# Performance work log

Hardware: AMD Instinct MI355X
Metric: run time of the kernel (lower is better)

Reference implementation:

```python
import jax, jax.numpy as jnp
import numpy as np

B, S_IN, T_OUT, H, L, V = 64, 512, 64, 1024, 2, 1024


def setup_inputs() -> dict:
    key = jax.random.key(0)
    ks = iter(jax.random.split(key, 64))
    def p(shape, scale=0.02):
        return (jax.random.normal(next(ks), shape, jnp.float32) * scale)
    d = {"x": jax.random.normal(next(ks), (B, 2, S_IN), jnp.float32)}
    d["emb"] = p((V, H))
    for l in range(L):
        i = 2 if l == 0 else H
        d[f"enc_Wih{l}"] = p((3 * H, i)); d[f"enc_Whh{l}"] = p((3 * H, H))
        d[f"enc_bih{l}"] = p((3 * H,));   d[f"enc_bhh{l}"] = p((3 * H,))
        d[f"dec_Wih{l}"] = p((H, H));     d[f"dec_Whh{l}"] = p((H, H))
        d[f"dec_bih{l}"] = p((H,));       d[f"dec_bhh{l}"] = p((H,))
    d["hq_W"] = p((H, H)); d["hq_b"] = p((H,))
    d["comb_W"] = p((H, 2 * H)); d["comb_b"] = p((H,))
    d["fc_W"] = p((V, H)); d["fc_b"] = p((V,))
    return d


def _gru_layer(x_seq, Wih, Whh, bih, bhh):
    # x_seq: [B,T,I] -> (outputs [B,T,H], h_T [B,H]). PyTorch GRU gate order r,z,n.
    xp = jnp.einsum('bti,gi->btg', x_seq, Wih) + bih  # [B,T,3H]
    h0 = jnp.zeros((x_seq.shape[0], Whh.shape[1]), x_seq.dtype)
    def step(h, xpt):
        hp = h @ Whh.T + bhh
        xr, xz, xn = jnp.split(xpt, 3, axis=-1)
        hr, hz, hn = jnp.split(hp, 3, axis=-1)
        r = jax.nn.sigmoid(xr + hr)
        z = jax.nn.sigmoid(xz + hz)
        n = jnp.tanh(xn + r * hn)
        h = (1.0 - z) * n + z * h
        return h, h
    hT, ys = jax.lax.scan(step, h0, jnp.swapaxes(xp, 0, 1))
    return jnp.swapaxes(ys, 0, 1), hT


def _forward(x, emb,
             enc_Wih0, enc_Whh0, enc_bih0, enc_bhh0,
             enc_Wih1, enc_Whh1, enc_bih1, enc_bhh1,
             dec_Wih0, dec_Whh0, dec_bih0, dec_bhh0,
             dec_Wih1, dec_Whh1, dec_bih1, dec_bhh1,
             hq_W, hq_b, comb_W, comb_b, fc_W, fc_b):
    enc_params = [(enc_Wih0, enc_Whh0, enc_bih0, enc_bhh0),
                  (enc_Wih1, enc_Whh1, enc_bih1, enc_bhh1)]
    dec_params = [(dec_Wih0, dec_Whh0, dec_bih0, dec_bhh0),
                  (dec_Wih1, dec_Whh1, dec_bih1, dec_bhh1)]
    # ---- encoder: GRU over x permuted to [B, S_in, 2] ----
    seq = jnp.transpose(x, (0, 2, 1)).astype(jnp.float32)
    h_enc = []
    for (Wih, Whh, bih, bhh) in enc_params:
        seq, hT = _gru_layer(seq, Wih, Whh, bih, bhh)
        h_enc.append(hT)
    enc_outs = seq                      # [B, S_in, H]
    hidden0 = jnp.stack(h_enc, axis=0)  # [L, B, H]

    tok0 = jnp.zeros((B,), jnp.int32)
    def dec_step(carry, _):
        tok, hid = carry
        inp = emb[tok]                  # [B, H]
        new_h = []
        for l, (Wih, Whh, bih, bhh) in enumerate(dec_params):
            h = jnp.tanh(inp @ Wih.T + bih + hid[l] @ Whh.T + bhh)
            new_h.append(h)
            inp = h
        hid = jnp.stack(new_h, axis=0)
        q = inp @ hq_W.T + hq_b                          # [B, H]
        scores = jnp.einsum('bsh,bh->bs', enc_outs, q)   # [B, S_in]
        aw = jax.nn.softmax(scores, axis=1)
        att = jnp.einsum('bs,bsh->bh', aw, enc_outs)     # [B, H]
        logits = jnp.concatenate([inp, att], axis=-1) @ comb_W.T + comb_b
        logits = logits @ fc_W.T + fc_b                  # [B, V]
        tok = jnp.argmax(logits, axis=-1).astype(jnp.int32)
        return (tok, hid), (logits, aw)
    (_, hidden), (logits_t, aw_t) = jax.lax.scan(dec_step, (tok0, hidden0), None, length=T_OUT)
    vec_out = jnp.swapaxes(logits_t, 0, 1)   # [B, T_out, V]
    attn = aw_t[-1][:, None, :]              # [B, 1, S_in] (last step, as in source)
    return vec_out, hidden, attn


def reference(x, emb,
              enc_Wih0, enc_Whh0, enc_bih0, enc_bhh0,
              enc_Wih1, enc_Whh1, enc_bih1, enc_bhh1,
              dec_Wih0, dec_Whh0, dec_bih0, dec_bhh0,
              dec_Wih1, dec_Whh1, dec_bih1, dec_bhh1,
              hq_W, hq_b, comb_W, comb_b, fc_W, fc_b):
    return _forward(x, emb,
                    enc_Wih0, enc_Whh0, enc_bih0, enc_bhh0,
                    enc_Wih1, enc_Whh1, enc_bih1, enc_bhh1,
                    dec_Wih0, dec_Whh0, dec_bih0, dec_bhh0,
                    dec_Wih1, dec_Whh1, dec_bih1, dec_bhh1,
                    hq_W, hq_b, comb_W, comb_b, fc_W, fc_b)
```

## Files before the change

kernel.cpp:

```cpp
#include <hip/hip_runtime.h>
#include <stdint.h>


#define BB 64
#define SS 512
#define TT 64
#define HH 1024
#define VV 1024
#define BH 65536
#define SH 524288
#define OFF_HID  4194304
#define OFF_ATTN 4325376

typedef _Float16 half8  __attribute__((ext_vector_type(8)));
typedef float    floatx4 __attribute__((ext_vector_type(4)));

struct P {
  const float *x, *emb;
  const float *eWih0, *eWhh0, *ebih0, *ebhh0;
  const float *dWih0, *dWhh0, *dbih0, *dbhh0;
  const float *eWih1, *eWhh1, *ebih1, *ebhh1;
  const float *dWih1, *dWhh1, *dbih1, *dbhh1;
  const float *hqW, *hqb, *combW, *combb, *fcW, *fcb;
  uint32_t* enc_i;
  _Float16 *W0h,*W0l;
  _Float16 *W1h,*W1l;
  _Float16 *embh,*embl,*T0h,*T0l;
  _Float16 *wih0dh,*wih0dl,*wih1dh,*wih1dl,*whh0dh,*whh0dl,*whh1dh,*whh1dl;
  _Float16 *hqh,*hql,*combh,*combl,*fch,*fcl;
  _Float16 *h0h,*h0l,*h1h,*h1l;
  _Float16 *dh0h,*dh0l,*dh1h,*dh1l;
  _Float16 *cath,*catl;
  _Float16 *ch,*cl;
  float *u0,*u1,*w1x,*q;
  float *attp_o;
  float *attp_ml;
  float *sc63;
  unsigned long long* amax;
  float* dout;
};

struct GSet { const _Float16 *Wh, *Wl, *Ah, *Al; const float *bias; float *out; };

__device__ __forceinline__ void splitf(float x, _Float16& hi, _Float16& lo){
  _Float16 h = (_Float16)x; hi = h;
  lo = (_Float16)((x - (float)h) * 2048.0f);
}
__device__ __forceinline__ float reconf(_Float16 hi, _Float16 lo){
  return fmaf((float)lo, 1.0f/2048.0f, (float)hi);
}
__device__ __forceinline__ float recon_u32(uint32_t w){
  float hi = (float)__builtin_bit_cast(_Float16, (unsigned short)(w & 0xffffu));
  float lo = (float)__builtin_bit_cast(_Float16, (unsigned short)(w >> 16));
  return fmaf(lo, 1.0f/2048.0f, hi);
}
__device__ __forceinline__ uint32_t pack_pair(float x){
  _Float16 hi, lo; splitf(x, hi, lo);
  return (uint32_t)__builtin_bit_cast(unsigned short, hi)
       | ((uint32_t)__builtin_bit_cast(unsigned short, lo) << 16);
}
__device__ __forceinline__ unsigned ordf(float f){
  unsigned u = __float_as_uint(f);
  return (u & 0x80000000u) ? ~u : (u | 0x80000000u);
}

template<int NT, int KH, bool SPLIT>
__device__ __forceinline__ void gemm_core(
    const _Float16* __restrict__ Ah0, const _Float16* __restrict__ Al0,
    const _Float16* __restrict__ Ah1, const _Float16* __restrict__ Al1,
    int sA,
    const _Float16* __restrict__ Wh, const _Float16* __restrict__ Wl,
    int nrows, _Float16* ldsW, float* accOut)
{
  const int tid = threadIdx.x, lane = tid & 63, wave = tid >> 6;
  const int mA = (wave<<4) + (lane & 15);
  const int kb = ((lane>>4) << 3);
  const int wstride = KH << 10;
  floatx4 aH[NT], aM1[NT], aM2[NT];
  int ne[NT];
  const _Float16* bh_base[NT];
  const _Float16* bl_base[NT];
  #pragma unroll
  for (int nt=0; nt<NT; ++nt){
    int nn = (lane & 15) + (nt<<4);
    ne[nt] = nn < nrows ? nn : nrows - 1;
    bh_base[nt] = ldsW + ne[nt]*1032 + kb;
    aH[nt]  = floatx4{0.f,0.f,0.f,0.f};
    aM1[nt] = floatx4{0.f,0.f,0.f,0.f};
    aM2[nt] = floatx4{0.f,0.f,0.f,0.f};
  }
  #pragma unroll
  for (int kh=0; kh<KH; ++kh){
    __syncthreads();
    const int iters = (nrows*128 + 255) >> 8;
    for (int it=0; it<iters; ++it){
      int idx = tid + (it<<8);
      int row = idx >> 7, col = (idx & 127) << 3;
      if (row < nrows)
        *(half8*)(ldsW + row*1032 + col) =
            *(const half8*)(Wh + row*wstride + (kh<<10) + col);
    }
    __syncthreads();
    const _Float16* ah_p = ((KH==2 && kh==1) ? Ah1 : Ah0) + mA*sA + kb;
    const _Float16* al_p = ((KH==2 && kh==1) ? Al1 : Al0) + mA*sA + kb;
    #pragma unroll
    for (int nt=0; nt<NT; ++nt) bl_base[nt] = Wl + ne[nt]*wstride + (kh<<10) + kb;
    #pragma unroll 4
    for (int ks=0; ks<32; ++ks){
      half8 ah = *(const half8*)(ah_p + (ks<<5));
      half8 al = *(const half8*)(al_p + (ks<<5));
      #pragma unroll
      for (int nt=0; nt<NT; ++nt){
        half8 bh = *(const half8*)(bh_base[nt] + (ks<<5));
        half8 bl = *(const half8*)(bl_base[nt] + (ks<<5));
        aH[nt]  = __builtin_amdgcn_mfma_f32_16x16x32_f16(ah, bh, aH[nt],  0,0,0);
        aM1[nt] = __builtin_amdgcn_mfma_f32_16x16x32_f16(ah, bl, aM1[nt], 0,0,0);
        aM2[nt] = __builtin_amdgcn_mfma_f32_16x16x32_f16(al, bh, aM2[nt], 0,0,0);
      }
    }
    if (SPLIT){
      #pragma unroll
      for (int nt=0; nt<NT; ++nt){
        #pragma unroll
        for (int r=0;r<4;++r)
          accOut[(kh*NT + nt)*4 + r] = aH[nt][r] + (aM1[nt][r] + aM2[nt][r]) * (1.f/2048.f);
        aH[nt]  = floatx4{0.f,0.f,0.f,0.f};
        aM1[nt] = floatx4{0.f,0.f,0.f,0.f};
        aM2[nt] = floatx4{0.f,0.f,0.f,0.f};
      }
    }
  }
  if (!SPLIT){
    #pragma unroll
    for (int nt=0; nt<NT; ++nt)
      #pragma unroll
      for (int r=0;r<4;++r)
        accOut[nt*4 + r] = aH[nt][r] + (aM1[nt][r] + aM2[nt][r]) * (1.f/2048.f);
  }
}

__global__ __launch_bounds__(256) void k_split(const float* __restrict__ src,
                                               _Float16* dh, _Float16* dl, int n){
  for (int i = blockIdx.x*256 + threadIdx.x; i < n; i += gridDim.x*256){
    _Float16 hi,lo; splitf(src[i],hi,lo); dh[i]=hi; dl[i]=lo;
  }
}

__global__ __launch_bounds__(256) void k_rw0(P p){
  const int n = 128*24*1024;
  for (int i = blockIdx.x*256 + threadIdx.x; i < n; i += gridDim.x*256){
    int k = i & 1023; int rest = i >> 10; int rr = rest % 24; int blk = rest / 24;
    int grow = (rr>>3)*1024 + (blk<<3) + (rr&7);
    _Float16 hi,lo; splitf(p.eWhh0[grow*1024 + k],hi,lo);
    p.W0h[i]=hi; p.W0l[i]=lo;
  }
}
__global__ __launch_bounds__(256) void k_rw1(P p){
  const int n = 128*24*2048;
  for (int i = blockIdx.x*256 + threadIdx.x; i < n; i += gridDim.x*256){
    int k = i & 2047; int rest = i >> 11; int rr = rest % 24; int blk = rest / 24;
    int grow = (rr>>3)*1024 + (blk<<3) + (rr&7);
    float v = (k < 1024) ? p.eWhh1[grow*1024 + k] : p.eWih1[grow*1024 + (k-1024)];
    _Float16 hi,lo; splitf(v,hi,lo);
    p.W1h[i]=hi; p.W1l[i]=lo;
  }
}
__global__ __launch_bounds__(256) void k_zero(P p){
  int i = blockIdx.x*256 + threadIdx.x;
  p.h1h[i] = (_Float16)0.f; p.h1l[i] = (_Float16)0.f;
  p.h0h[BH + i] = (_Float16)0.f; p.h0l[BH + i] = (_Float16)0.f;
}
__global__ __launch_bounds__(256) void k_t0(P p){
  __shared__ _Float16 ldsW[16*1032];
  const int ns = blockIdx.x & 63, mc = blockIdx.x >> 6;
  float acc[4];
  gemm_core<1,1,false>(p.embh + mc*65536, p.embl + mc*65536, nullptr, nullptr, 1024,
                       p.wih0dh + ns*16*1024, p.wih0dl + ns*16*1024, 16, ldsW, acc);
  const int lane = threadIdx.x & 63, wave = threadIdx.x >> 6;
  const int n = lane & 15, col = (ns<<4) + n;
  const float bv = p.dbih0[col];
  #pragma unroll
  for (int r=0;r<4;++r){
    int v = mc*64 + (wave<<4) + ((lane>>4)<<2) + r;
    _Float16 hi,lo; splitf(acc[r] + bv, hi, lo);
    p.T0h[v*1024 + col] = hi; p.T0l[v*1024 + col] = lo;
  }
}

__global__ __launch_bounds__(256) void k_enc(P p, int e){
  const int tid = threadIdx.x, lane = tid & 63, wave = tid >> 6;
  const bool is0 = blockIdx.x < 128;
  if (is0 && e >= 512) return;
  if (!is0 && e < 1) return;
  const int blk = is0 ? blockIdx.x : blockIdx.x - 128;
  const int j0 = blk << 3;

  __shared__ _Float16 ldsW[24*1032];
  __shared__ float ldsG[2][24][68];
  __shared__ float ldsC[24][4];

  if (tid < 24){
    int grow = (tid>>3)*1024 + j0 + (tid & 7);
    if (is0){
      ldsC[tid][0] = p.eWih0[grow*2+0];
      ldsC[tid][1] = p.eWih0[grow*2+1];
      ldsC[tid][2] = p.ebih0[grow];
      ldsC[tid][3] = p.ebhh0[grow];
    } else {
      ldsC[tid][0] = p.ebih1[grow];
      ldsC[tid][1] = p.ebhh1[grow];
    }
  }

  const int cur = e & 1, prv = cur ^ 1;
  float acc[16];
  if (is0){
    gemm_core<2,1,true>(p.h0h + prv*BH, p.h0l + prv*BH, nullptr, nullptr, 1024,
                        p.W0h + blk*24*1024, p.W0l + blk*24*1024, 24, ldsW, acc);
    #pragma unroll
    for (int nt=0; nt<2; ++nt){
      int n = (lane & 15) + (nt<<4);
      if (n < 24){
        #pragma unroll
        for (int r=0;r<4;++r)
          ldsG[0][n][(wave<<4)+((lane>>4)<<2)+r] = acc[nt*4+r];
      }
    }
  } else {
    gemm_core<2,2,true>(p.h1h + prv*BH, p.h1l + prv*BH,
                        p.h0h + prv*BH, p.h0l + prv*BH, 1024,
                        p.W1h + blk*24*2048, p.W1l + blk*24*2048, 24, ldsW, acc);
    #pragma unroll
    for (int kh=0; kh<2; ++kh){
      #pragma unroll
      for (int nt=0; nt<2; ++nt){
        int n = (lane & 15) + (nt<<4);
        if (n < 24){
          #pragma unroll
          for (int r=0;r<4;++r)
            ldsG[kh][n][(wave<<4)+((lane>>4)<<2)+r] = acc[(kh*2+nt)*4+r];
        }
      }
    }
  }
  __syncthreads();

  #pragma unroll
  for (int it=0; it<2; ++it){
    int idx = tid + (it<<8);
    int b = idx & 63, j = idx >> 6;
    int col = j0 + j;
    if (is0){
      int t = e;
      float hr = ldsG[0][j][b]    + ldsC[j][3];
      float hz = ldsG[0][8+j][b]  + ldsC[8+j][3];
      float hn = ldsG[0][16+j][b] + ldsC[16+j][3];
      float x0 = p.x[b*1024 + t], x1 = p.x[b*1024 + 512 + t];
      float xr = fmaf(x0, ldsC[j][0],    fmaf(x1, ldsC[j][1],    ldsC[j][2]));
      float xz = fmaf(x0, ldsC[8+j][0],  fmaf(x1, ldsC[8+j][1],  ldsC[8+j][2]));
      float xn = fmaf(x0, ldsC[16+j][0], fmaf(x1, ldsC[16+j][1], ldsC[16+j][2]));
      float rg = 1.0f/(1.0f + expf(-(xr+hr)));
      float zg = 1.0f/(1.0f + expf(-(xz+hz)));
      float ng = tanhf(xn + rg*hn);
      float hold = reconf(p.h0h[prv*BH + b*1024 + col], p.h0l[prv*BH + b*1024 + col]);
      float hnew = (1.0f - zg)*ng + zg*hold;
      _Float16 hi,lo; splitf(hnew,hi,lo);
      p.h0h[cur*BH + b*1024 + col] = hi;
      p.h0l[cur*BH + b*1024 + col] = lo;
    } else {
      int t = e - 1;
      float hr = ldsG[0][j][b]    + ldsC[j][1];
      float hz = ldsG[0][8+j][b]  + ldsC[8+j][1];
      float hn = ldsG[0][16+j][b] + ldsC[16+j][1];
      float xr = ldsG[1][j][b]    + ldsC[j][0];
      float xz = ldsG[1][8+j][b]  + ldsC[8+j][0];
      float xn = ldsG[1][16+j][b] + ldsC[16+j][0];
      float rg = 1.0f/(1.0f + expf(-(xr+hr)));
      float zg = 1.0f/(1.0f + expf(-(xz+hz)));
      float ng = tanhf(xn + rg*hn);
      float hold = reconf(p.h1h[prv*BH + b*1024 + col], p.h1l[prv*BH + b*1024 + col]);
      float hnew = (1.0f - zg)*ng + zg*hold;
      _Float16 hi,lo; splitf(hnew,hi,lo);
      p.h1h[cur*BH + b*1024 + col] = hi;
      p.h1l[cur*BH + b*1024 + col] = lo;
      p.enc_i[b*SH + t*1024 + col] = pack_pair(hnew);
    }
  }
}

__global__ __launch_bounds__(256) void k_dgemm2(GSet a, GSet b){
  const int tid = threadIdx.x, lane = tid & 63, wave = tid >> 6;
  const GSet g = blockIdx.x < 128 ? a : b;
  const int blk = blockIdx.x & 127;
  __shared__ _Float16 ldsW[8*1032];
  float acc[4];
  gemm_core<1,1,false>(g.Ah, g.Al, nullptr, nullptr, 1024,
                       g.Wh + blk*8*1024, g.Wl + blk*8*1024, 8, ldsW, acc);
  int n = lane & 15;
  if (n < 8){
    int col = (blk<<3) + n;
    float bv = g.bias[col];
    #pragma unroll
    for (int r=0;r<4;++r){
      int m = (wave<<4)+((lane>>4)<<2)+r;
      g.out[m*1024 + col] = acc[r] + bv;
    }
  }
}

__global__ __launch_bounds__(256) void k_dec0(P p, int t){
  const int tid = threadIdx.x, b = blockIdx.x;
  __shared__ unsigned long long red[256];
  unsigned long long v = 0;
  if (t > 0 && tid < 128) v = p.amax[b*128 + tid];
  red[tid] = v; __syncthreads();
  for (int off=128; off>=1; off>>=1){
    if (tid < off){ unsigned long long o = red[tid+off]; if (o > red[tid]) red[tid] = o; }
    __syncthreads();
  }
  const int tokb = (t > 0) ? (1023 - (int)(red[0] & 0xffffffffULL)) : 0;
  #pragma unroll
  for (int i=0;i<4;++i){
    int h = tid + (i<<8);
    float val = tanhf(reconf(p.T0h[tokb*1024+h], p.T0l[tokb*1024+h]) + p.u0[b*1024+h]);
    _Float16 hi,lo; splitf(val,hi,lo);
    p.dh0h[b*1024+h]=hi; p.dh0l[b*1024+h]=lo;
  }
}
__global__ __launch_bounds__(256) void k_dec2(P p){
  const int tid = threadIdx.x, b = blockIdx.x;
  #pragma unroll
  for (int i=0;i<4;++i){
    int h = tid + (i<<8);
    float val = tanhf(p.w1x[b*1024+h] + p.u1[b*1024+h]);
    _Float16 hi,lo; splitf(val,hi,lo);
    p.dh1h[b*1024+h]=hi; p.dh1l[b*1024+h]=lo;
    p.cath[b*2048+h]=hi; p.catl[b*2048+h]=lo;
  }
}
__global__ __launch_bounds__(256) void k_flash(P p, int t){
  const int tid = threadIdx.x, lane = tid & 63, wave = tid >> 6;
  const int b = blockIdx.x >> 1, half = blockIdx.x & 1;
  const int s0 = half << 8;
  const bool last = (t == 63);
  float qv[16];
  #pragma unroll
  for (int i=0;i<16;++i) qv[i] = p.q[b*1024 + (i<<6) + lane];
  float ov[16];
  #pragma unroll
  for (int i=0;i<16;++i) ov[i] = 0.f;
  float mrun = -3.0e38f, lrun = 0.f;
  for (int si=0; si<64; ++si){
    int s = s0 + (wave<<6) + si;
    const uint32_t* ep = p.enc_i + b*SH + s*1024 + lane;
    float ef[16]; float partial = 0.f;
    #pragma unroll
    for (int i=0;i<16;++i){
      ef[i] = recon_u32(ep[i<<6]);
      partial = fmaf(ef[i], qv[i], partial);
    }
    #pragma unroll
    for (int off=32; off; off>>=1) partial += __shfl_xor(partial, off, 64);
    if (last && lane == 0) p.sc63[b*512 + s] = partial;
    float mnew = fmaxf(mrun, partial);
    float fac = __expf(mrun - mnew);
    float w   = __expf(partial - mnew);
    lrun = fmaf(lrun, fac, w);
    #pragma unroll
    for (int i=0;i<16;++i) ov[i] = fmaf(ov[i], fac, w*ef[i]);
    mrun = mnew;
  }
  __shared__ float ldsO[4][1024];
  __shared__ float ldsM[4], ldsL2[4];
  #pragma unroll
  for (int i=0;i<16;++i) ldsO[wave][(i<<6)+lane] = ov[i];
  if (lane == 0){ ldsM[wave] = mrun; ldsL2[wave] = lrun; }
  __syncthreads();
  float M = fmaxf(fmaxf(ldsM[0],ldsM[1]), fmaxf(ldsM[2],ldsM[3]));
  float f0 = __expf(ldsM[0]-M), f1 = __expf(ldsM[1]-M),
        f2 = __expf(ldsM[2]-M), f3 = __expf(ldsM[3]-M);
  if (tid == 0){
    p.attp_ml[b*4 + half*2 + 0] = M;
    p.attp_ml[b*4 + half*2 + 1] = f0*ldsL2[0] + f1*ldsL2[1] + f2*ldsL2[2] + f3*ldsL2[3];
  }
  #pragma unroll
  for (int i=0;i<4;++i){
    int h = tid + (i<<8);
    p.attp_o[(b*2+half)*1024 + h] =
        f0*ldsO[0][h] + f1*ldsO[1][h] + f2*ldsO[2][h] + f3*ldsO[3][h];
  }
}
__global__ __launch_bounds__(256) void k_dec5(P p, int t){
  const int tid = threadIdx.x, b = blockIdx.x;
  float m0 = p.attp_ml[b*4+0], l0 = p.attp_ml[b*4+1];
  float m1 = p.attp_ml[b*4+2], l1 = p.attp_ml[b*4+3];
  float M = fmaxf(m0,m1);
  float f0 = expf(m0-M), f1 = expf(m1-M);
  float invL = 1.0f/(f0*l0 + f1*l1);
  #pragma unroll
  for (int i=0;i<4;++i){
    int h = tid + (i<<8);
    float o = (f0*p.attp_o[(b*2+0)*1024+h] + f1*p.attp_o[(b*2+1)*1024+h]) * invL;
    _Float16 hi,lo; splitf(o,hi,lo);
    p.cath[b*2048 + 1024 + h] = hi; p.catl[b*2048 + 1024 + h] = lo;
  }
  if (t == 63){
    #pragma unroll
    for (int i=0;i<2;++i){
      int s = tid + (i<<8);
      p.dout[OFF_ATTN + b*512 + s] = expf(p.sc63[b*512+s] - M) * invL;
    }
  }
}
__global__ __launch_bounds__(256) void k_comb(P p){
  const int tid = threadIdx.x, lane = tid & 63, wave = tid >> 6;
  const int blk = blockIdx.x;
  __shared__ _Float16 ldsW[8*1032];
  float acc[4];
  gemm_core<1,2,false>(p.cath, p.catl, p.cath + 1024, p.catl + 1024, 2048,
                       p.combh + blk*8*2048, p.combl + blk*8*2048, 8, ldsW, acc);
  int n = lane & 15;
  if (n < 8){
    int col = (blk<<3) + n;
    float bv = p.combb[col];
    #pragma unroll
    for (int r=0;r<4;++r){
      int m = (wave<<4)+((lane>>4)<<2)+r;
      _Float16 hi,lo; splitf(acc[r] + bv, hi, lo);
      p.ch[m*1024 + col] = hi; p.cl[m*1024 + col] = lo;
    }
  }
}
__global__ __launch_bounds__(256) void k_fc(P p, int t){
  const int tid = threadIdx.x, lane = tid & 63, wave = tid >> 6;
  const int blk = blockIdx.x;
  __shared__ _Float16 ldsW[8*1032];
  __shared__ float ldsL[8][68];
  float acc[4];
  gemm_core<1,1,false>(p.ch, p.cl, nullptr, nullptr, 1024,
                       p.fch + blk*8*1024, p.fcl + blk*8*1024, 8, ldsW, acc);
  int n = lane & 15;
  if (n < 8){
    int col = (blk<<3) + n;
    float bv = p.fcb[col];
    #pragma unroll
    for (int r=0;r<4;++r){
      int m = (wave<<4)+((lane>>4)<<2)+r;
      float val = acc[r] + bv;
      p.dout[m*65536 + t*1024 + col] = val;
      ldsL[n][m] = val;
    }
  }
  __syncthreads();
  if (tid < 64){
    int b = tid; float best = -3.0e38f; int bi = 0;
    #pragma unroll
    for (int jj=0; jj<8; ++jj){
      float v = ldsL[jj][b];
      if (v > best){ best = v; bi = jj; }
    }
    unsigned long long pk = ((unsigned long long)ordf(best) << 32)
                          | (unsigned)(1023 - ((blk<<3) + bi));
    p.amax[b*128 + blk] = pk;
  }
}
__global__ __launch_bounds__(256) void k_hidden(P p){
  int idx = blockIdx.x*256 + threadIdx.x;
  int i = idx & 65535;
  float v = (idx >> 16) ? reconf(p.dh1h[i], p.dh1l[i]) : reconf(p.dh0h[i], p.dh0l[i]);
  p.dout[OFF_HID + idx] = v;
}

extern "C" void kernel_launch(void* const* d_in, const int* in_sizes, int n_in,
                              void* d_out, int out_size, void* d_ws, size_t ws_size,
                              hipStream_t stream)
{
  (void)in_sizes; (void)n_in; (void)out_size;
  P p;
  p.x     = (const float*)d_in[0];  p.emb   = (const float*)d_in[1];
  p.eWih0 = (const float*)d_in[2];  p.eWhh0 = (const float*)d_in[3];
  p.ebih0 = (const float*)d_in[4];  p.ebhh0 = (const float*)d_in[5];
  p.dWih0 = (const float*)d_in[6];  p.dWhh0 = (const float*)d_in[7];
  p.dbih0 = (const float*)d_in[8];  p.dbhh0 = (const float*)d_in[9];
  p.eWih1 = (const float*)d_in[10]; p.eWhh1 = (const float*)d_in[11];
  p.ebih1 = (const float*)d_in[12]; p.ebhh1 = (const float*)d_in[13];
  p.dWih1 = (const float*)d_in[14]; p.dWhh1 = (const float*)d_in[15];
  p.dbih1 = (const float*)d_in[16]; p.dbhh1 = (const float*)d_in[17];
  p.hqW   = (const float*)d_in[18]; p.hqb   = (const float*)d_in[19];
  p.combW = (const float*)d_in[20]; p.combb = (const float*)d_in[21];
  p.fcW   = (const float*)d_in[22]; p.fcb   = (const float*)d_in[23];
  p.dout  = (float*)d_out;

  char* base = (char*)d_ws; size_t off = 0;
  auto alloc = [&](size_t bytes)->char*{
    char* r = base + off; off = (off + bytes + 255) & ~(size_t)255; return r;
  };
  p.enc_i = (uint32_t*)alloc(33554432ULL*4);
  p.W0h = (_Float16*)alloc(3145728ULL*2);  p.W0l = (_Float16*)alloc(3145728ULL*2);
  p.W1h = (_Float16*)alloc(6291456ULL*2);  p.W1l = (_Float16*)alloc(6291456ULL*2);
  p.embh = (_Float16*)alloc(1048576ULL*2); p.embl = (_Float16*)alloc(1048576ULL*2);
  p.T0h  = (_Float16*)alloc(1048576ULL*2); p.T0l  = (_Float16*)alloc(1048576ULL*2);
  p.wih0dh=(_Float16*)alloc(1048576ULL*2); p.wih0dl=(_Float16*)alloc(1048576ULL*2);
  p.wih1dh=(_Float16*)alloc(1048576ULL*2); p.wih1dl=(_Float16*)alloc(1048576ULL*2);
  p.whh0dh=(_Float16*)alloc(1048576ULL*2); p.whh0dl=(_Float16*)alloc(1048576ULL*2);
  p.whh1dh=(_Float16*)alloc(1048576ULL*2); p.whh1dl=(_Float16*)alloc(1048576ULL*2);
  p.hqh  = (_Float16*)alloc(1048576ULL*2); p.hql  = (_Float16*)alloc(1048576ULL*2);
  p.combh= (_Float16*)alloc(2097152ULL*2); p.combl= (_Float16*)alloc(2097152ULL*2);
  p.fch  = (_Float16*)alloc(1048576ULL*2); p.fcl  = (_Float16*)alloc(1048576ULL*2);
  p.h0h  = (_Float16*)alloc(131072ULL*2);  p.h0l  = (_Float16*)alloc(131072ULL*2);
  p.h1h  = (_Float16*)alloc(131072ULL*2);  p.h1l  = (_Float16*)alloc(131072ULL*2);
  p.dh0h = (_Float16*)alloc(65536ULL*2);   p.dh0l = (_Float16*)alloc(65536ULL*2);
  p.dh1h = (_Float16*)alloc(65536ULL*2);   p.dh1l = (_Float16*)alloc(65536ULL*2);
  p.cath = (_Float16*)alloc(131072ULL*2);  p.catl = (_Float16*)alloc(131072ULL*2);
  p.ch   = (_Float16*)alloc(65536ULL*2);   p.cl   = (_Float16*)alloc(65536ULL*2);
  p.u0   = (float*)alloc(65536ULL*4);      p.u1   = (float*)alloc(65536ULL*4);
  p.w1x  = (float*)alloc(65536ULL*4);      p.q    = (float*)alloc(65536ULL*4);
  p.attp_o  = (float*)alloc(131072ULL*4);
  p.attp_ml = (float*)alloc(256ULL*4);
  p.sc63    = (float*)alloc(32768ULL*4);
  p.amax    = (unsigned long long*)alloc(8192ULL*8);
  if (off > ws_size) return;

  k_split<<<2048,256,0,stream>>>(p.emb,   p.embh,   p.embl,   1048576);
  k_split<<<2048,256,0,stream>>>(p.dWih0, p.wih0dh, p.wih0dl, 1048576);
  k_split<<<2048,256,0,stream>>>(p.dWih1, p.wih1dh, p.wih1dl, 1048576);
  k_split<<<2048,256,0,stream>>>(p.dWhh0, p.whh0dh, p.whh0dl, 1048576);
  k_split<<<2048,256,0,stream>>>(p.dWhh1, p.whh1dh, p.whh1dl, 1048576);
  k_split<<<2048,256,0,stream>>>(p.hqW,   p.hqh,    p.hql,    1048576);
  k_split<<<2048,256,0,stream>>>(p.combW, p.combh,  p.combl,  2097152);
  k_split<<<2048,256,0,stream>>>(p.fcW,   p.fch,    p.fcl,    1048576);
  k_rw0<<<4096,256,0,stream>>>(p);
  k_rw1<<<4096,256,0,stream>>>(p);
  k_zero<<<256,256,0,stream>>>(p);
  k_t0<<<1024,256,0,stream>>>(p);

  for (int e=0; e<=512; ++e) k_enc<<<256,256,0,stream>>>(p, e);

  {
    GSet a{p.whh0dh, p.whh0dl, p.h0h + BH, p.h0l + BH, p.dbhh0, p.u0};
    GSet b{p.whh1dh, p.whh1dl, p.h1h,      p.h1l,      p.dbhh1, p.u1};
    k_dgemm2<<<256,256,0,stream>>>(a, b);
  }
  GSet sK1a{p.wih1dh, p.wih1dl, p.dh0h, p.dh0l, p.dbih1, p.w1x};
  GSet sK1b{p.whh0dh, p.whh0dl, p.dh0h, p.dh0l, p.dbhh0, p.u0};
  GSet sK3a{p.hqh,    p.hql,    p.dh1h, p.dh1l, p.hqb,   p.q};
  GSet sK3b{p.whh1dh, p.whh1dl, p.dh1h, p.dh1l, p.dbhh1, p.u1};

  for (int t=0; t<64; ++t){
    k_dec0<<<64,256,0,stream>>>(p, t);
    k_dgemm2<<<256,256,0,stream>>>(sK1a, sK1b);
    k_dec2<<<64,256,0,stream>>>(p);
    k_dgemm2<<<256,256,0,stream>>>(sK3a, sK3b);
    k_flash<<<128,256,0,stream>>>(p, t);
    k_dec5<<<64,256,0,stream>>>(p, t);
    k_comb<<<128,256,0,stream>>>(p);
    k_fc<<<128,256,0,stream>>>(p, t);
  }
  k_hidden<<<512,256,0,stream>>>(p);
}
```

Before: 30.20 ms.

## Convert per-step encoder/decoder launches into persistent kernels with grid barriers

```diff
diff --git a/kernel.cpp b/kernel.cpp
--- a/kernel.cpp
+++ b/kernel.cpp
@@ -32,15 +32,14 @@
   _Float16 *dh0h,*dh0l,*dh1h,*dh1l;
   _Float16 *cath,*catl;
   _Float16 *ch,*cl;
-  float *u0,*u1,*w1x,*q;
+  float *u0,*u1,*q;
   float *attp_o;
   float *attp_ml;
   float *sc63;
   unsigned long long* amax;
+  unsigned *bar0, *bar1;
   float* dout;
 };
-
-struct GSet { const _Float16 *Wh, *Wl, *Ah, *Al; const float *bias; float *out; };
 
 __device__ __forceinline__ void splitf(float x, _Float16& hi, _Float16& lo){
   _Float16 h = (_Float16)x; hi = h;
@@ -62,6 +61,18 @@
 __device__ __forceinline__ unsigned ordf(float f){
   unsigned u = __float_as_uint(f);
   return (u & 0x80000000u) ? ~u : (u | 0x80000000u);
+}
+
+__device__ __forceinline__ void gbar(unsigned* c, unsigned target){
+  __syncthreads();
+  if (threadIdx.x == 0){
+    __threadfence();
+    __hip_atomic_fetch_add(c, 1u, __ATOMIC_RELAXED, __HIP_MEMORY_SCOPE_AGENT);
+    while (__hip_atomic_load(c, __ATOMIC_RELAXED, __HIP_MEMORY_SCOPE_AGENT) < target)
+      __builtin_amdgcn_s_sleep(4);
+    __threadfence();
+  }
+  __syncthreads();
 }
 
 template<int NT, int KH, bool SPLIT>
@@ -139,10 +150,19 @@
   }
 }
 
-__global__ __launch_bounds__(256) void k_split(const float* __restrict__ src,
-                                               _Float16* dh, _Float16* dl, int n){
-  for (int i = blockIdx.x*256 + threadIdx.x; i < n; i += gridDim.x*256){
-    _Float16 hi,lo; splitf(src[i],hi,lo); dh[i]=hi; dl[i]=lo;
+__global__ __launch_bounds__(256) void k_splitall(P p){
+  const int M = 1<<20;
+  for (int i = blockIdx.x*256 + threadIdx.x; i < 9*M; i += gridDim.x*256){
+    const float* s; _Float16 *dh, *dl; int j;
+    if      (i <   M){ j=i;     s=p.emb;   dh=p.embh;   dl=p.embl; }
+    else if (i < 2*M){ j=i-M;   s=p.dWih0; dh=p.wih0dh; dl=p.wih0dl; }
+    else if (i < 3*M){ j=i-2*M; s=p.dWih1; dh=p.wih1dh; dl=p.wih1dl; }
+    else if (i < 4*M){ j=i-3*M; s=p.dWhh0; dh=p.whh0dh; dl=p.whh0dl; }
+    else if (i < 5*M){ j=i-4*M; s=p.dWhh1; dh=p.whh1dh; dl=p.whh1dl; }
+    else if (i < 6*M){ j=i-5*M; s=p.hqW;   dh=p.hqh;    dl=p.hql; }
+    else if (i < 8*M){ j=i-6*M; s=p.combW; dh=p.combh;  dl=p.combl; }
+    else             { j=i-8*M; s=p.fcW;   dh=p.fch;    dl=p.fcl; }
+    _Float16 hi,lo; splitf(s[j],hi,lo); dh[j]=hi; dl[j]=lo;
   }
 }
 
@@ -169,6 +189,7 @@
   int i = blockIdx.x*256 + threadIdx.x;
   p.h1h[i] = (_Float16)0.f; p.h1l[i] = (_Float16)0.f;
   p.h0h[BH + i] = (_Float16)0.f; p.h0l[BH + i] = (_Float16)0.f;
+  if (i == 0){ *p.bar0 = 0u; *p.bar1 = 0u; }
 }
 __global__ __launch_bounds__(256) void k_t0(P p){
   __shared__ _Float16 ldsW[16*1032];
@@ -187,288 +208,396 @@
   }
 }
 
-__global__ __launch_bounds__(256) void k_enc(P p, int e){
+template<int KSIT>
+__device__ __forceinline__ void frag2(
+    const _Float16* __restrict__ a0h, const _Float16* __restrict__ a0l,
+    const _Float16* __restrict__ a1h, const _Float16* __restrict__ a1l,
+    const _Float16* __restrict__ b0h, const _Float16* __restrict__ b0l,
+    const _Float16* __restrict__ b1h, const _Float16* __restrict__ b1l,
+    float* o)
+{
+  floatx4 H00{0,0,0,0},H10{0,0,0,0},H01{0,0,0,0},H11{0,0,0,0};
+  floatx4 M00{0,0,0,0},M10{0,0,0,0},M01{0,0,0,0},M11{0,0,0,0};
+  floatx4 N00{0,0,0,0},N10{0,0,0,0},N01{0,0,0,0},N11{0,0,0,0};
+  #pragma unroll
+  for (int ks=0; ks<KSIT; ++ks){
+    const int off = ks<<5;
+    half8 A0h = *(const half8*)(a0h+off), A0l = *(const half8*)(a0l+off);
+    half8 A1h = *(const half8*)(a1h+off), A1l = *(const half8*)(a1l+off);
+    half8 B0h = *(const half8*)(b0h+off), B0l = *(const half8*)(b0l+off);
+    half8 B1h = *(const half8*)(b1h+off), B1l = *(const half8*)(b1l+off);
+    H00 = __builtin_amdgcn_mfma_f32_16x16x32_f16(A0h,B0h,H00,0,0,0);
+    M00 = __builtin_amdgcn_mfma_f32_16x16x32_f16(A0h,B0l,M00,0,0,0);
+    N00 = __builtin_amdgcn_mfma_f32_16x16x32_f16(A0l,B0h,N00,0,0,0);
+    H10 = __builtin_amdgcn_mfma_f32_16x16x32_f16(A1h,B0h,H10,0,0,0);
+    M10 = __builtin_amdgcn_mfma_f32_16x16x32_f16(A1h,B0l,M10,0,0,0);
+    N10 = __builtin_amdgcn_mfma_f32_16x16x32_f16(A1l,B0h,N10,0,0,0);
+    H01 = __builtin_amdgcn_mfma_f32_16x16x32_f16(A0h,B1h,H01,0,0,0);
+    M01 = __builtin_amdgcn_mfma_f32_16x16x32_f16(A0h,B1l,M01,0,0,0);
+    N01 = __builtin_amdgcn_mfma_f32_16x16x32_f16(A0l,B1h,N01,0,0,0);
+    H11 = __builtin_amdgcn_mfma_f32_16x16x32_f16(A1h,B1h,H11,0,0,0);
+    M11 = __builtin_amdgcn_mfma_f32_16x16x32_f16(A1h,B1l,M11,0,0,0);
+    N11 = __builtin_amdgcn_mfma_f32_16x16x32_f16(A1l,B1h,N11,0,0,0);
+  }
+  const float s = 1.f/2048.f;
+  #pragma unroll
+  for (int r=0;r<4;++r){
+    o[r]    = H00[r] + (M00[r]+N00[r])*s;
+    o[4+r]  = H10[r] + (M10[r]+N10[r])*s;
+    o[8+r]  = H01[r] + (M01[r]+N01[r])*s;
+    o[12+r] = H11[r] + (M11[r]+N11[r])*s;
+  }
+}
+
+__global__ __launch_bounds__(1024) void k_encp(P p){
   const int tid = threadIdx.x, lane = tid & 63, wave = tid >> 6;
+  const int mtg = wave & 1, kg = wave >> 1;
   const bool is0 = blockIdx.x < 128;
-  if (is0 && e >= 512) return;
-  if (!is0 && e < 1) return;
-  const int blk = is0 ? blockIdx.x : blockIdx.x - 128;
+  const int blk = is0 ? (int)blockIdx.x : (int)blockIdx.x - 128;
   const int j0 = blk << 3;
-
-  __shared__ _Float16 ldsW[24*1032];
-  __shared__ float ldsG[2][24][68];
+  __shared__ float ldsA[8][24][68];
   __shared__ float ldsC[24][4];
-
   if (tid < 24){
     int grow = (tid>>3)*1024 + j0 + (tid & 7);
-    if (is0){
-      ldsC[tid][0] = p.eWih0[grow*2+0];
-      ldsC[tid][1] = p.eWih0[grow*2+1];
-      ldsC[tid][2] = p.ebih0[grow];
-      ldsC[tid][3] = p.ebhh0[grow];
-    } else {
-      ldsC[tid][0] = p.ebih1[grow];
-      ldsC[tid][1] = p.ebhh1[grow];
-    }
-  }
-
-  const int cur = e & 1, prv = cur ^ 1;
-  float acc[16];
+    if (is0){ ldsC[tid][0]=p.eWih0[grow*2]; ldsC[tid][1]=p.eWih0[grow*2+1];
+              ldsC[tid][2]=p.ebih0[grow];   ldsC[tid][3]=p.ebhh0[grow]; }
+    else    { ldsC[tid][0]=p.ebih1[grow];   ldsC[tid][1]=p.ebhh1[grow]; }
+  }
+
+  const int ln15 = lane & 15, kb = (lane >> 4) << 3;
+  const int m0 = (mtg << 5) + ln15;
+  const int ne1 = ln15 < 8 ? 16 + ln15 : 23;
+
+  const _Float16 *b0h,*b0l,*b1h,*b1l, *a0h0,*a0l0;
   if (is0){
-    gemm_core<2,1,true>(p.h0h + prv*BH, p.h0l + prv*BH, nullptr, nullptr, 1024,
-                        p.W0h + blk*24*1024, p.W0l + blk*24*1024, 24, ldsW, acc);
-    #pragma unroll
-    for (int nt=0; nt<2; ++nt){
-      int n = (lane & 15) + (nt<<4);
-      if (n < 24){
-        #pragma unroll
-        for (int r=0;r<4;++r)
-          ldsG[0][n][(wave<<4)+((lane>>4)<<2)+r] = acc[nt*4+r];
-      }
-    }
+    const int ks0 = kg << 7;
+    const _Float16* wbh = p.W0h + (size_t)blk*24*1024;
+    const _Float16* wbl = p.W0l + (size_t)blk*24*1024;
+    b0h = wbh + ln15*1024 + ks0 + kb;  b0l = wbl + ln15*1024 + ks0 + kb;
+    b1h = wbh + ne1 *1024 + ks0 + kb;  b1l = wbl + ne1 *1024 + ks0 + kb;
+    a0h0 = p.h0h + m0*1024 + ks0 + kb;
+    a0l0 = p.h0l + m0*1024 + ks0 + kb;
   } else {
-    gemm_core<2,2,true>(p.h1h + prv*BH, p.h1l + prv*BH,
-                        p.h0h + prv*BH, p.h0l + prv*BH, 1024,
-                        p.W1h + blk*24*2048, p.W1l + blk*24*2048, 24, ldsW, acc);
-    #pragma unroll
-    for (int kh=0; kh<2; ++kh){
-      #pragma unroll
-      for (int nt=0; nt<2; ++nt){
-        int n = (lane & 15) + (nt<<4);
-        if (n < 24){
-          #pragma unroll
-          for (int r=0;r<4;++r)
-            ldsG[kh][n][(wave<<4)+((lane>>4)<<2)+r] = acc[(kh*2+nt)*4+r];
+    const int ks0 = kg << 8;
+    const _Float16* wbh = p.W1h + (size_t)blk*24*2048;
+    const _Float16* wbl = p.W1l + (size_t)blk*24*2048;
+    b0h = wbh + ln15*2048 + ks0 + kb;  b0l = wbl + ln15*2048 + ks0 + kb;
+    b1h = wbh + ne1 *2048 + ks0 + kb;  b1l = wbl + ne1 *2048 + ks0 + kb;
+    const _Float16* hh = (kg < 4) ? p.h1h : p.h0h;
+    const _Float16* hl = (kg < 4) ? p.h1l : p.h0l;
+    const int aoff = ((kg & 3) << 8) + kb;
+    a0h0 = hh + m0*1024 + aoff;
+    a0l0 = hl + m0*1024 + aoff;
+  }
+  const _Float16 *a1h0 = a0h0 + (16*1024), *a1l0 = a0l0 + (16*1024);
+
+  #pragma unroll 1
+  for (int e = 0; e <= 512; ++e){
+    const int cur = e & 1, prv = cur ^ 1;
+    const bool active = is0 ? (e < 512) : (e >= 1);
+    if (active){
+      const int po = prv * BH;
+      float o[16];
+      if (is0) frag2<4>(a0h0+po, a0l0+po, a1h0+po, a1l0+po, b0h,b0l,b1h,b1l, o);
+      else     frag2<8>(a0h0+po, a0l0+po, a1h0+po, a1l0+po, b0h,b0l,b1h,b1l, o);
+      #pragma unroll
+      for (int mti=0; mti<2; ++mti){
+        const int mcol = (((mtg<<1)+mti)<<4) + ((lane>>4)<<2);
+        #pragma unroll
+        for (int r=0;r<4;++r){
+          ldsA[kg][ln15][mcol+r] = o[mti*4+r];
+          if (ln15 < 8) ldsA[kg][16+ln15][mcol+r] = o[8+mti*4+r];
         }
       }
     }
-  }
-  __syncthreads();
-
+    __syncthreads();
+    if (active && tid < 512){
+      const int b = tid & 63, j = tid >> 6;
+      const int col = j0 + j;
+      float sr=0.f, sz=0.f, sn=0.f;
+      if (is0){
+        #pragma unroll
+        for (int k=0;k<8;++k){ sr += ldsA[k][j][b]; sz += ldsA[k][8+j][b]; sn += ldsA[k][16+j][b]; }
+        const int t = e;
+        float hr = sr + ldsC[j][3], hz = sz + ldsC[8+j][3], hn = sn + ldsC[16+j][3];
+        float x0 = p.x[b*1024 + t], x1 = p.x[b*1024 + 512 + t];
+        float xr = fmaf(x0, ldsC[j][0],    fmaf(x1, ldsC[j][1],    ldsC[j][2]));
+        float xz = fmaf(x0, ldsC[8+j][0],  fmaf(x1, ldsC[8+j][1],  ldsC[8+j][2]));
+        float xn = fmaf(x0, ldsC[16+j][0], fmaf(x1, ldsC[16+j][1], ldsC[16+j][2]));
+        float rg = 1.0f/(1.0f + expf(-(xr+hr)));
+        float zg = 1.0f/(1.0f + expf(-(xz+hz)));
+        float ng = tanhf(xn + rg*hn);
+        float hold = reconf(p.h0h[prv*BH + b*1024 + col], p.h0l[prv*BH + b*1024 + col]);
+        float hnew = (1.0f - zg)*ng + zg*hold;
+        _Float16 hi,lo; splitf(hnew,hi,lo);
+        p.h0h[cur*BH + b*1024 + col] = hi;
+        p.h0l[cur*BH + b*1024 + col] = lo;
+      } else {
+        float xr4=0.f, xz4=0.f, xn4=0.f;
+        #pragma unroll
+        for (int k=0;k<4;++k){
+          sr  += ldsA[k][j][b];   sz  += ldsA[k][8+j][b];   sn  += ldsA[k][16+j][b];
+          xr4 += ldsA[4+k][j][b]; xz4 += ldsA[4+k][8+j][b]; xn4 += ldsA[4+k][16+j][b];
+        }
+        const int t = e - 1;
+        float hr = sr + ldsC[j][1],  hz = sz + ldsC[8+j][1],  hn = sn + ldsC[16+j][1];
+        float xr = xr4 + ldsC[j][0], xz = xz4 + ldsC[8+j][0], xn = xn4 + ldsC[16+j][0];
+        float rg = 1.0f/(1.0f + expf(-(xr+hr)));
+        float zg = 1.0f/(1.0f + expf(-(xz+hz)));
+        float ng = tanhf(xn + rg*hn);
+        float hold = reconf(p.h1h[prv*BH + b*1024 + col], p.h1l[prv*BH + b*1024 + col]);
+        float hnew = (1.0f - zg)*ng + zg*hold;
+        _Float16 hi,lo; splitf(hnew,hi,lo);
+        p.h1h[cur*BH + b*1024 + col] = hi;
+        p.h1l[cur*BH + b*1024 + col] = lo;
+        p.enc_i[b*SH + t*1024 + col] = pack_pair(hnew);
+      }
+    }
+    gbar(p.bar0, (unsigned)(e+1) << 8);
+  }
+}
+
+template<int K>
+__device__ __forceinline__ void dec_mm(int tid,
+    const _Float16* __restrict__ Ah, const _Float16* __restrict__ Al,
+    const _Float16* __restrict__ Wh, const _Float16* __restrict__ Wl,
+    float (*ldsD)[8][68])
+{
+  const int lane = tid & 63, wave = tid >> 6;
+  const int mtg = wave & 1, kg = wave >> 1;
+  const int ln15 = lane & 15, kb = (lane>>4)<<3;
+  const int ks0 = kg * (K/4);
+  const int ne = ln15 < 8 ? ln15 : 7;
+  const _Float16* a0h = Ah + (mtg*32 + ln15)*K + ks0 + kb;
+  const _Float16* a0l = Al + (mtg*32 + ln15)*K + ks0 + kb;
+  const _Float16* a1h = a0h + 16*K;
+  const _Float16* a1l = a0l + 16*K;
+  const _Float16* wh = Wh + ne*K + ks0 + kb;
+  const _Float16* wl = Wl + ne*K + ks0 + kb;
+  floatx4 H0{0,0,0,0},M0{0,0,0,0},N0{0,0,0,0},H1{0,0,0,0},M1{0,0,0,0},N1{0,0,0,0};
   #pragma unroll
-  for (int it=0; it<2; ++it){
-    int idx = tid + (it<<8);
-    int b = idx & 63, j = idx >> 6;
-    int col = j0 + j;
-    if (is0){
-      int t = e;
-      float hr = ldsG[0][j][b]    + ldsC[j][3];
-      float hz = ldsG[0][8+j][b]  + ldsC[8+j][3];
-      float hn = ldsG[0][16+j][b] + ldsC[16+j][3];
-      float x0 = p.x[b*1024 + t], x1 = p.x[b*1024 + 512 + t];
-      float xr = fmaf(x0, ldsC[j][0],    fmaf(x1, ldsC[j][1],    ldsC[j][2]));
-      float xz = fmaf(x0, ldsC[8+j][0],  fmaf(x1, ldsC[8+j][1],  ldsC[8+j][2]));
-      float xn = fmaf(x0, ldsC[16+j][0], fmaf(x1, ldsC[16+j][1], ldsC[16+j][2]));
-      float rg = 1.0f/(1.0f + expf(-(xr+hr)));
-      float zg = 1.0f/(1.0f + expf(-(xz+hz)));
-      float ng = tanhf(xn + rg*hn);
-      float hold = reconf(p.h0h[prv*BH + b*1024 + col], p.h0l[prv*BH + b*1024 + col]);
-      float hnew = (1.0f - zg)*ng + zg*hold;
-      _Float16 hi,lo; splitf(hnew,hi,lo);
-      p.h0h[cur*BH + b*1024 + col] = hi;
-      p.h0l[cur*BH + b*1024 + col] = lo;
-    } else {
-      int t = e - 1;
-      float hr = ldsG[0][j][b]    + ldsC[j][1];
-      float hz = ldsG[0][8+j][b]  + ldsC[8+j][1];
-      float hn = ldsG[0][16+j][b] + ldsC[16+j][1];
-      float xr = ldsG[1][j][b]    + ldsC[j][0];
-      float xz = ldsG[1][8+j][b]  + ldsC[8+j][0];
-      float xn = ldsG[1][16+j][b] + ldsC[16+j][0];
-      float rg = 1.0f/(1.0f + expf(-(xr+hr)));
-      float zg = 1.0f/(1.0f + expf(-(xz+hz)));
-      float ng = tanhf(xn + rg*hn);
-      float hold = reconf(p.h1h[prv*BH + b*1024 + col], p.h1l[prv*BH + b*1024 + col]);
-      float hnew = (1.0f - zg)*ng + zg*hold;
-      _Float16 hi,lo; splitf(hnew,hi,lo);
-      p.h1h[cur*BH + b*1024 + col] = hi;
-      p.h1l[cur*BH + b*1024 + col] = lo;
-      p.enc_i[b*SH + t*1024 + col] = pack_pair(hnew);
-    }
-  }
-}
-
-__global__ __launch_bounds__(256) void k_dgemm2(GSet a, GSet b){
-  const int tid = threadIdx.x, lane = tid & 63, wave = tid >> 6;
-  const GSet g = blockIdx.x < 128 ? a : b;
-  const int blk = blockIdx.x & 127;
-  __shared__ _Float16 ldsW[8*1032];
-  float acc[4];
-  gemm_core<1,1,false>(g.Ah, g.Al, nullptr, nullptr, 1024,
-                       g.Wh + blk*8*1024, g.Wl + blk*8*1024, 8, ldsW, acc);
-  int n = lane & 15;
-  if (n < 8){
-    int col = (blk<<3) + n;
-    float bv = g.bias[col];
+  for (int ks=0; ks<K/128; ++ks){
+    const int off = ks<<5;
+    half8 A0h = *(const half8*)(a0h+off), A0l = *(const half8*)(a0l+off);
+    half8 A1h = *(const half8*)(a1h+off), A1l = *(const half8*)(a1l+off);
+    half8 Bh  = *(const half8*)(wh+off),  Bl  = *(const half8*)(wl+off);
+    H0 = __builtin_amdgcn_mfma_f32_16x16x32_f16(A0h,Bh,H0,0,0,0);
+    M0 = __builtin_amdgcn_mfma_f32_16x16x32_f16(A0h,Bl,M0,0,0,0);
+    N0 = __builtin_amdgcn_mfma_f32_16x16x32_f16(A0l,Bh,N0,0,0,0);
+    H1 = __builtin_amdgcn_mfma_f32_16x16x32_f16(A1h,Bh,H1,0,0,0);
+    M1 = __builtin_amdgcn_mfma_f32_16x16x32_f16(A1h,Bl,M1,0,0,0);
+    N1 = __builtin_amdgcn_mfma_f32_16x16x32_f16(A1l,Bh,N1,0,0,0);
+  }
+  if (ln15 < 8){
+    const float s = 1.f/2048.f;
+    const int mc = mtg*32 + ((lane>>4)<<2);
     #pragma unroll
     for (int r=0;r<4;++r){
-      int m = (wave<<4)+((lane>>4)<<2)+r;
-      g.out[m*1024 + col] = acc[r] + bv;
-    }
-  }
-}
-
-__global__ __launch_bounds__(256) void k_dec0(P p, int t){
-  const int tid = threadIdx.x, b = blockIdx.x;
-  __shared__ unsigned long long red[256];
-  unsigned long long v = 0;
-  if (t > 0 && tid < 128) v = p.amax[b*128 + tid];
-  red[tid] = v; __syncthreads();
-  for (int off=128; off>=1; off>>=1){
-    if (tid < off){ unsigned long long o = red[tid+off]; if (o > red[tid]) red[tid] = o; }
+      ldsD[kg][ln15][mc+r]    = H0[r] + (M0[r]+N0[r])*s;
+      ldsD[kg][ln15][mc+16+r] = H1[r] + (M1[r]+N1[r])*s;
+    }
+  }
+}
+
+__global__ __launch_bounds__(512) void k_decp(P p){
+  const int tid = threadIdx.x, lane = tid & 63, wave = tid >> 6;
+  const int bid = blockIdx.x;
+  __shared__ float sbuf[8][1032];
+  __shared__ float ldsD[4][8][68];
+  __shared__ float ldsL[8][68];
+  __shared__ float sml[16];
+  __shared__ unsigned long long sred[128];
+  unsigned ph = 0;
+
+  {
+    const bool A = bid < 128; const int blk = bid & 127;
+    const _Float16* Wh = A ? p.whh0dh : p.whh1dh;
+    const _Float16* Wl = A ? p.whh0dl : p.whh1dl;
+    const _Float16* Ah = A ? (p.h0h + BH) : p.h1h;
+    const _Float16* Al = A ? (p.h0l + BH) : p.h1l;
+    dec_mm<1024>(tid, Ah, Al, Wh + (size_t)blk*8*1024, Wl + (size_t)blk*8*1024, ldsD);
     __syncthreads();
-  }
-  const int tokb = (t > 0) ? (1023 - (int)(red[0] & 0xffffffffULL)) : 0;
-  #pragma unroll
-  for (int i=0;i<4;++i){
-    int h = tid + (i<<8);
-    float val = tanhf(reconf(p.T0h[tokb*1024+h], p.T0l[tokb*1024+h]) + p.u0[b*1024+h]);
-    _Float16 hi,lo; splitf(val,hi,lo);
-    p.dh0h[b*1024+h]=hi; p.dh0l[b*1024+h]=lo;
-  }
-}
-__global__ __launch_bounds__(256) void k_dec2(P p){
-  const int tid = threadIdx.x, b = blockIdx.x;
-  #pragma unroll
-  for (int i=0;i<4;++i){
-    int h = tid + (i<<8);
-    float val = tanhf(p.w1x[b*1024+h] + p.u1[b*1024+h]);
-    _Float16 hi,lo; splitf(val,hi,lo);
-    p.dh1h[b*1024+h]=hi; p.dh1l[b*1024+h]=lo;
-    p.cath[b*2048+h]=hi; p.catl[b*2048+h]=lo;
-  }
-}
-__global__ __launch_bounds__(256) void k_flash(P p, int t){
-  const int tid = threadIdx.x, lane = tid & 63, wave = tid >> 6;
-  const int b = blockIdx.x >> 1, half = blockIdx.x & 1;
-  const int s0 = half << 8;
-  const bool last = (t == 63);
-  float qv[16];
-  #pragma unroll
-  for (int i=0;i<16;++i) qv[i] = p.q[b*1024 + (i<<6) + lane];
-  float ov[16];
-  #pragma unroll
-  for (int i=0;i<16;++i) ov[i] = 0.f;
-  float mrun = -3.0e38f, lrun = 0.f;
-  for (int si=0; si<64; ++si){
-    int s = s0 + (wave<<6) + si;
-    const uint32_t* ep = p.enc_i + b*SH + s*1024 + lane;
-    float ef[16]; float partial = 0.f;
-    #pragma unroll
-    for (int i=0;i<16;++i){
-      ef[i] = recon_u32(ep[i<<6]);
-      partial = fmaf(ef[i], qv[i], partial);
-    }
-    #pragma unroll
-    for (int off=32; off; off>>=1) partial += __shfl_xor(partial, off, 64);
-    if (last && lane == 0) p.sc63[b*512 + s] = partial;
-    float mnew = fmaxf(mrun, partial);
-    float fac = __expf(mrun - mnew);
-    float w   = __expf(partial - mnew);
-    lrun = fmaf(lrun, fac, w);
-    #pragma unroll
-    for (int i=0;i<16;++i) ov[i] = fmaf(ov[i], fac, w*ef[i]);
-    mrun = mnew;
-  }
-  __shared__ float ldsO[4][1024];
-  __shared__ float ldsM[4], ldsL2[4];
-  #pragma unroll
-  for (int i=0;i<16;++i) ldsO[wave][(i<<6)+lane] = ov[i];
-  if (lane == 0){ ldsM[wave] = mrun; ldsL2[wave] = lrun; }
-  __syncthreads();
-  float M = fmaxf(fmaxf(ldsM[0],ldsM[1]), fmaxf(ldsM[2],ldsM[3]));
-  float f0 = __expf(ldsM[0]-M), f1 = __expf(ldsM[1]-M),
-        f2 = __expf(ldsM[2]-M), f3 = __expf(ldsM[3]-M);
-  if (tid == 0){
-    p.attp_ml[b*4 + half*2 + 0] = M;
-    p.attp_ml[b*4 + half*2 + 1] = f0*ldsL2[0] + f1*ldsL2[1] + f2*ldsL2[2] + f3*ldsL2[3];
-  }
-  #pragma unroll
-  for (int i=0;i<4;++i){
-    int h = tid + (i<<8);
-    p.attp_o[(b*2+half)*1024 + h] =
-        f0*ldsO[0][h] + f1*ldsO[1][h] + f2*ldsO[2][h] + f3*ldsO[3][h];
-  }
-}
-__global__ __launch_bounds__(256) void k_dec5(P p, int t){
-  const int tid = threadIdx.x, b = blockIdx.x;
-  float m0 = p.attp_ml[b*4+0], l0 = p.attp_ml[b*4+1];
-  float m1 = p.attp_ml[b*4+2], l1 = p.attp_ml[b*4+3];
-  float M = fmaxf(m0,m1);
-  float f0 = expf(m0-M), f1 = expf(m1-M);
-  float invL = 1.0f/(f0*l0 + f1*l1);
-  #pragma unroll
-  for (int i=0;i<4;++i){
-    int h = tid + (i<<8);
-    float o = (f0*p.attp_o[(b*2+0)*1024+h] + f1*p.attp_o[(b*2+1)*1024+h]) * invL;
-    _Float16 hi,lo; splitf(o,hi,lo);
-    p.cath[b*2048 + 1024 + h] = hi; p.catl[b*2048 + 1024 + h] = lo;
-  }
-  if (t == 63){
-    #pragma unroll
-    for (int i=0;i<2;++i){
-      int s = tid + (i<<8);
-      p.dout[OFF_ATTN + b*512 + s] = expf(p.sc63[b*512+s] - M) * invL;
-    }
-  }
-}
-__global__ __launch_bounds__(256) void k_comb(P p){
-  const int tid = threadIdx.x, lane = tid & 63, wave = tid >> 6;
-  const int blk = blockIdx.x;
-  __shared__ _Float16 ldsW[8*1032];
-  float acc[4];
-  gemm_core<1,2,false>(p.cath, p.catl, p.cath + 1024, p.catl + 1024, 2048,
-                       p.combh + blk*8*2048, p.combl + blk*8*2048, 8, ldsW, acc);
-  int n = lane & 15;
-  if (n < 8){
-    int col = (blk<<3) + n;
-    float bv = p.combb[col];
-    #pragma unroll
-    for (int r=0;r<4;++r){
-      int m = (wave<<4)+((lane>>4)<<2)+r;
-      _Float16 hi,lo; splitf(acc[r] + bv, hi, lo);
-      p.ch[m*1024 + col] = hi; p.cl[m*1024 + col] = lo;
-    }
-  }
-}
-__global__ __launch_bounds__(256) void k_fc(P p, int t){
-  const int tid = threadIdx.x, lane = tid & 63, wave = tid >> 6;
-  const int blk = blockIdx.x;
-  __shared__ _Float16 ldsW[8*1032];
-  __shared__ float ldsL[8][68];
-  float acc[4];
-  gemm_core<1,1,false>(p.ch, p.cl, nullptr, nullptr, 1024,
-                       p.fch + blk*8*1024, p.fcl + blk*8*1024, 8, ldsW, acc);
-  int n = lane & 15;
-  if (n < 8){
-    int col = (blk<<3) + n;
-    float bv = p.fcb[col];
-    #pragma unroll
-    for (int r=0;r<4;++r){
-      int m = (wave<<4)+((lane>>4)<<2)+r;
-      float val = acc[r] + bv;
-      p.dout[m*65536 + t*1024 + col] = val;
-      ldsL[n][m] = val;
-    }
-  }
-  __syncthreads();
-  if (tid < 64){
-    int b = tid; float best = -3.0e38f; int bi = 0;
-    #pragma unroll
-    for (int jj=0; jj<8; ++jj){
-      float v = ldsL[jj][b];
-      if (v > best){ best = v; bi = jj; }
-    }
-    unsigned long long pk = ((unsigned long long)ordf(best) << 32)
-                          | (unsigned)(1023 - ((blk<<3) + bi));
-    p.amax[b*128 + blk] = pk;
-  }
-}
-__global__ __launch_bounds__(256) void k_hidden(P p){
-  int idx = blockIdx.x*256 + threadIdx.x;
-  int i = idx & 65535;
-  float v = (idx >> 16) ? reconf(p.dh1h[i], p.dh1l[i]) : reconf(p.dh0h[i], p.dh0l[i]);
-  p.dout[OFF_HID + idx] = v;
+    {
+      const int b = tid & 63, j = tid >> 6, col = (blk<<3) + j;
+      float val = ldsD[0][j][b]+ldsD[1][j][b]+ldsD[2][j][b]+ldsD[3][j][b]
+                + (A ? p.dbhh0 : p.dbhh1)[col];
+      (A ? p.u0 : p.u1)[b*1024 + col] = val;
+    }
+    ++ph; gbar(p.bar1, ph<<8);
+  }
+
+  #pragma unroll 1
+  for (int t=0; t<64; ++t){
+    if (bid < 64){
+      const int b = bid;
+      unsigned long long v = 0;
+      if (t > 0 && tid < 128) v = p.amax[b*128 + tid];
+      if (tid < 128) sred[tid] = v;
+      __syncthreads();
+      for (int off=64; off>=1; off>>=1){
+        if (tid < off){ unsigned long long o = sred[tid+off]; if (o > sred[tid]) sred[tid] = o; }
+        __syncthreads();
+      }
+      const int tok = (t > 0) ? (1023 - (int)(sred[0] & 0xffffffffULL)) : 0;
+      #pragma unroll
+      for (int i=0;i<2;++i){
+        int h = tid + (i<<9);
+        float val = tanhf(reconf(p.T0h[tok*1024+h], p.T0l[tok*1024+h]) + p.u0[b*1024+h]);
+        _Float16 hi,lo; splitf(val,hi,lo);
+        p.dh0h[b*1024+h]=hi; p.dh0l[b*1024+h]=lo;
+      }
+    }
+    ++ph; gbar(p.bar1, ph<<8);
+
+    {
+      const bool A = bid < 128; const int blk = bid & 127;
+      const _Float16* Wh = A ? p.wih1dh : p.whh0dh;
+      const _Float16* Wl = A ? p.wih1dl : p.whh0dl;
+      dec_mm<1024>(tid, p.dh0h, p.dh0l, Wh + (size_t)blk*8*1024, Wl + (size_t)blk*8*1024, ldsD);
+      __syncthreads();
+      const int b = tid & 63, j = tid >> 6, col = (blk<<3) + j;
+      float val = ldsD[0][j][b]+ldsD[1][j][b]+ldsD[2][j][b]+ldsD[3][j][b];
+      if (A){
+        float h1 = tanhf(val + p.dbih1[col] + p.u1[b*1024+col]);
+        _Float16 hi,lo; splitf(h1,hi,lo);
+        p.dh1h[b*1024+col]=hi; p.dh1l[b*1024+col]=lo;
+        p.cath[b*2048+col]=hi; p.catl[b*2048+col]=lo;
+      } else {
+        p.u0[b*1024+col] = val + p.dbhh0[col];
+      }
+    }
+    ++ph; gbar(p.bar1, ph<<8);
+
+    {
+      const bool A = bid < 128; const int blk = bid & 127;
+      const _Float16* Wh = A ? p.hqh : p.whh1dh;
+      const _Float16* Wl = A ? p.hql : p.whh1dl;
+      dec_mm<1024>(tid, p.dh1h, p.dh1l, Wh + (size_t)blk*8*1024, Wl + (size_t)blk*8*1024, ldsD);
+      __syncthreads();
+      const int b = tid & 63, j = tid >> 6, col = (blk<<3) + j;
+      float val = ldsD[0][j][b]+ldsD[1][j][b]+ldsD[2][j][b]+ldsD[3][j][b];
+      if (A) p.q[b*1024+col]  = val + p.hqb[col];
+      else   p.u1[b*1024+col] = val + p.dbhh1[col];
+    }
+    ++ph; gbar(p.bar1, ph<<8);
+
+    {
+      const int b = bid >> 2, q4 = bid & 3;
+      const int s0 = q4 << 7;
+      float qv[16];
+      #pragma unroll
+      for (int i=0;i<16;++i) qv[i] = p.q[b*1024 + (i<<6) + lane];
+      float ov[16];
+      #pragma unroll
+      for (int i=0;i<16;++i) ov[i] = 0.f;
+      float mrun = -3.0e38f, lrun = 0.f;
+      for (int si=0; si<16; ++si){
+        int s = s0 + (wave<<4) + si;
+        const uint32_t* ep = p.enc_i + b*SH + s*1024 + lane;
+        float ef[16]; float partial = 0.f;
+        #pragma unroll
+        for (int i=0;i<16;++i){
+          ef[i] = recon_u32(ep[i<<6]);
+          partial = fmaf(ef[i], qv[i], partial);
+        }
+        #pragma unroll
+        for (int off=32; off; off>>=1) partial += __shfl_xor(partial, off, 64);
+        if (t == 63 && lane == 0) p.sc63[b*512 + s] = partial;
+        float mnew = fmaxf(mrun, partial);
+        float fac = __expf(mrun - mnew);
+        float w   = __expf(partial - mnew);
+        lrun = fmaf(lrun, fac, w);
+        #pragma unroll
+        for (int i=0;i<16;++i) ov[i] = fmaf(ov[i], fac, w*ef[i]);
+        mrun = mnew;
+      }
+      #pragma unroll
+      for (int i=0;i<16;++i) sbuf[wave][(i<<6)+lane] = ov[i];
+      if (lane == 0){ sml[wave] = mrun; sml[8+wave] = lrun; }
+      __syncthreads();
+      float M = sml[0];
+      #pragma unroll
+      for (int w=1;w<8;++w) M = fmaxf(M, sml[w]);
+      float fw[8], L = 0.f;
+      #pragma unroll
+      for (int w=0;w<8;++w){ fw[w] = __expf(sml[w]-M); L += fw[w]*sml[8+w]; }
+      if (tid == 0){ p.attp_ml[(b*4+q4)*2] = M; p.attp_ml[(b*4+q4)*2+1] = L; }
+      #pragma unroll
+      for (int i=0;i<2;++i){
+        int h = tid + (i<<9);
+        float o = 0.f;
+        #pragma unroll
+        for (int w=0;w<8;++w) o += fw[w]*sbuf[w][h];
+        p.attp_o[(b*4+q4)*1024 + h] = o;
+      }
+    }
+    ++ph; gbar(p.bar1, ph<<8);
+
+    if (bid < 64){
+      const int b = bid;
+      float m0=p.attp_ml[b*8+0], l0=p.attp_ml[b*8+1];
+      float m1=p.attp_ml[b*8+2], l1=p.attp_ml[b*8+3];
+      float m2=p.attp_ml[b*8+4], l2=p.attp_ml[b*8+5];
+      float m3=p.attp_ml[b*8+6], l3=p.attp_ml[b*8+7];
+      float M = fmaxf(fmaxf(m0,m1), fmaxf(m2,m3));
+      float f0=expf(m0-M), f1=expf(m1-M), f2=expf(m2-M), f3=expf(m3-M);
+      float invL = 1.0f/(f0*l0 + f1*l1 + f2*l2 + f3*l3);
+      #pragma unroll
+      for (int i=0;i<2;++i){
+        int h = tid + (i<<9);
+        float o = (f0*p.attp_o[(b*4+0)*1024+h] + f1*p.attp_o[(b*4+1)*1024+h]
+                 + f2*p.attp_o[(b*4+2)*1024+h] + f3*p.attp_o[(b*4+3)*1024+h]) * invL;
+        _Float16 hi,lo; splitf(o,hi,lo);
+        p.cath[b*2048 + 1024 + h] = hi; p.catl[b*2048 + 1024 + h] = lo;
+      }
+      if (t == 63){
+        int s = tid;
+        p.dout[OFF_ATTN + b*512 + s] = expf(p.sc63[b*512+s] - M) * invL;
+      }
+    }
+    ++ph; gbar(p.bar1, ph<<8);
+
+    if (bid < 128){
+      dec_mm<2048>(tid, p.cath, p.catl,
+                   p.combh + (size_t)bid*8*2048, p.combl + (size_t)bid*8*2048, ldsD);
+      __syncthreads();
+      const int b = tid & 63, j = tid >> 6, col = (bid<<3) + j;
+      float val = ldsD[0][j][b]+ldsD[1][j][b]+ldsD[2][j][b]+ldsD[3][j][b] + p.combb[col];
+      _Float16 hi,lo; splitf(val,hi,lo);
+      p.ch[b*1024+col]=hi; p.cl[b*1024+col]=lo;
+    }
+    ++ph; gbar(p.bar1, ph<<8);
+
+    if (bid < 128){
+      dec_mm<1024>(tid, p.ch, p.cl,
+                   p.fch + (size_t)bid*8*1024, p.fcl + (size_t)bid*8*1024, ldsD);
+      __syncthreads();
+      const int b = tid & 63, j = tid >> 6, col = (bid<<3) + j;
+      float val = ldsD[0][j][b]+ldsD[1][j][b]+ldsD[2][j][b]+ldsD[3][j][b] + p.fcb[col];
+      p.dout[b*65536 + t*1024 + col] = val;
+      ldsL[j][b] = val;
+      __syncthreads();
+      if (tid < 64){
+        int b2 = tid; float best = -3.0e38f; int bi = 0;
+        #pragma unroll
+        for (int jj=0; jj<8; ++jj){
+          float v = ldsL[jj][b2];
+          if (v > best){ best = v; bi = jj; }
+        }
+        unsigned long long pk = ((unsigned long long)ordf(best) << 32)
+                              | (unsigned)(1023 - ((bid<<3) + bi));
+        p.amax[b2*128 + bid] = pk;
+      }
+    }
+    ++ph; gbar(p.bar1, ph<<8);
+  }
+
+  {
+    int idx = bid*512 + tid;
+    int i = idx & 65535;
+    float v = (idx >> 16) ? reconf(p.dh1h[i], p.dh1l[i]) : reconf(p.dh0h[i], p.dh0l[i]);
+    p.dout[OFF_HID + idx] = v;
+  }
 }
 
 extern "C" void kernel_launch(void* const* d_in, const int* in_sizes, int n_in,
@@ -514,47 +643,22 @@
   p.cath = (_Float16*)alloc(131072ULL*2);  p.catl = (_Float16*)alloc(131072ULL*2);
   p.ch   = (_Float16*)alloc(65536ULL*2);   p.cl   = (_Float16*)alloc(65536ULL*2);
   p.u0   = (float*)alloc(65536ULL*4);      p.u1   = (float*)alloc(65536ULL*4);
-  p.w1x  = (float*)alloc(65536ULL*4);      p.q    = (float*)alloc(65536ULL*4);
-  p.attp_o  = (float*)alloc(131072ULL*4);
-  p.attp_ml = (float*)alloc(256ULL*4);
+  p.q    = (float*)alloc(65536ULL*4);
+  p.attp_o  = (float*)alloc(262144ULL*4);
+  p.attp_ml = (float*)alloc(512ULL*4);
   p.sc63    = (float*)alloc(32768ULL*4);
   p.amax    = (unsigned long long*)alloc(8192ULL*8);
+  {
+    unsigned* bars = (unsigned*)alloc(256);
+    p.bar0 = bars; p.bar1 = bars + 16;
+  }
   if (off > ws_size) return;
 
-  k_split<<<2048,256,0,stream>>>(p.emb,   p.embh,   p.embl,   1048576);
-  k_split<<<2048,256,0,stream>>>(p.dWih0, p.wih0dh, p.wih0dl, 1048576);
-  k_split<<<2048,256,0,stream>>>(p.dWih1, p.wih1dh, p.wih1dl, 1048576);
-  k_split<<<2048,256,0,stream>>>(p.dWhh0, p.whh0dh, p.whh0dl, 1048576);
-  k_split<<<2048,256,0,stream>>>(p.dWhh1, p.whh1dh, p.whh1dl, 1048576);
-  k_split<<<2048,256,0,stream>>>(p.hqW,   p.hqh,    p.hql,    1048576);
-  k_split<<<2048,256,0,stream>>>(p.combW, p.combh,  p.combl,  2097152);
-  k_split<<<2048,256,0,stream>>>(p.fcW,   p.fch,    p.fcl,    1048576);
+  k_splitall<<<4096,256,0,stream>>>(p);
   k_rw0<<<4096,256,0,stream>>>(p);
   k_rw1<<<4096,256,0,stream>>>(p);
   k_zero<<<256,256,0,stream>>>(p);
   k_t0<<<1024,256,0,stream>>>(p);
-
-  for (int e=0; e<=512; ++e) k_enc<<<256,256,0,stream>>>(p, e);
-
-  {
-    GSet a{p.whh0dh, p.whh0dl, p.h0h + BH, p.h0l + BH, p.dbhh0, p.u0};
-    GSet b{p.whh1dh, p.whh1dl, p.h1h,      p.h1l,      p.dbhh1, p.u1};
-    k_dgemm2<<<256,256,0,stream>>>(a, b);
-  }
-  GSet sK1a{p.wih1dh, p.wih1dl, p.dh0h, p.dh0l, p.dbih1, p.w1x};
-  GSet sK1b{p.whh0dh, p.whh0dl, p.dh0h, p.dh0l, p.dbhh0, p.u0};
-  GSet sK3a{p.hqh,    p.hql,    p.dh1h, p.dh1l, p.hqb,   p.q};
-  GSet sK3b{p.whh1dh, p.whh1dl, p.dh1h, p.dh1l, p.dbhh1, p.u1};
-
-  for (int t=0; t<64; ++t){
-    k_dec0<<<64,256,0,stream>>>(p, t);
-    k_dgemm2<<<256,256,0,stream>>>(sK1a, sK1b);
-    k_dec2<<<64,256,0,stream>>>(p);
-    k_dgemm2<<<256,256,0,stream>>>(sK3a, sK3b);
-    k_flash<<<128,256,0,stream>>>(p, t);
-    k_dec5<<<64,256,0,stream>>>(p, t);
-    k_comb<<<128,256,0,stream>>>(p);
-    k_fc<<<128,256,0,stream>>>(p, t);
-  }
-  k_hidden<<<512,256,0,stream>>>(p);
-}
+  k_encp<<<256,1024,0,stream>>>(p);
+  k_decp<<<256,512,0,stream>>>(p);
+}
```

Result: slower. 46.23 ms (+53.1%).
